# Optimization experiments

Measured on AMD Instinct MI355X. Metric: run time of the kernel, lower is better.

## Reference

```python
import jax, jax.numpy as jnp
import numpy as np

B, T, IN, H, C = 128, 128, 75, 512, 60


def setup_inputs() -> dict:
    key = jax.random.key(0)
    ks = jax.random.split(key, 40)
    def n(k, shape, s=0.05):
        return jax.random.normal(k, shape, dtype=jnp.float32) * s
    p = {}
    p["inputs"] = jax.random.normal(ks[0], (B, T, IN), dtype=jnp.float32)
    p["epoch"] = 1
    # three used LSTMCells: lstm_cell_t, lstm_cell (spatial), lstm_cell1
    i = 1
    for nm, isz in [("t", IN), ("s", IN), ("1", IN)]:
        p[f"Wih_{nm}"] = n(ks[i], (4 * H, isz)); i += 1
        p[f"Whh_{nm}"] = n(ks[i], (4 * H, H)); i += 1
        p[f"bih_{nm}"] = n(ks[i], (4 * H,)); i += 1
        p[f"bhh_{nm}"] = n(ks[i], (4 * H,)); i += 1
    p["fc_w"] = n(ks[i], (C, H)); i += 1
    p["fc_b"] = n(ks[i], (C,)); i += 1
    p["fct_w"] = n(ks[i], (H, IN)); i += 1
    p["fct_b"] = n(ks[i], (H,)); i += 1
    p["fc1_w"] = n(ks[i], (H, IN)); i += 1
    p["fc1_b"] = n(ks[i], (H,)); i += 1
    p["fc2_w"] = n(ks[i], (IN // 3, H)); i += 1
    p["fc2_b"] = n(ks[i], (IN // 3,)); i += 1
    p["W_x_t"] = n(ks[i], (H, H)); i += 1
    p["W_h_t"] = n(ks[i], (H, H)); i += 1
    p["b_t"] = n(ks[i], (H,)); i += 1
    p["W_x_s"] = n(ks[i], (H, H)); i += 1
    p["W_h_s"] = n(ks[i], (H, H)); i += 1
    p["U_s"] = n(ks[i], (H, H)); i += 1
    p["b_s"] = n(ks[i], (H,)); i += 1
    p["b_us"] = n(ks[i], (H,)); i += 1
    return p


def reference(inputs, epoch,
              Wih_t, Whh_t, bih_t, bhh_t,
              Wih_s, Whh_s, bih_s, bhh_s,
              Wih_1, Whh_1, bih_1, bhh_1,
              fc_w, fc_b, fct_w, fct_b, fc1_w, fc1_b, fc2_w, fc2_b,
              W_x_t, W_h_t, b_t, W_x_s, W_h_s, U_s, b_s, b_us):
    def cell(x, h, c, Wih, Whh, bih, bhh):
        g = x @ Wih.T + bih + h @ Whh.T + bhh            # [B, 4H]
        i, f, gg, o = jnp.split(g, 4, axis=1)
        c2 = jax.nn.sigmoid(f) * c + jax.nn.sigmoid(i) * jnp.tanh(gg)
        return jax.nn.sigmoid(o) * jnp.tanh(c2), c2

    def step(carry, x):  # x: [B, IN]
        hn_t, cn_t, hn_s, cn_s, hn1, cn1 = carry
        h_prev_t = hn_t
        hn_t, cn_t = cell(x, hn_t, cn_t, Wih_t, Whh_t, bih_t, bhh_t)
        # temporal gate beta (note: original adds BOTH b_s and b_t)
        beta = jax.nn.relu((x @ fct_w.T + fct_b) @ W_x_t + h_prev_t @ W_h_t + b_s + b_t)
        h_prev = hn_s
        hn_s, cn_s = cell(x, hn_s, cn_s, Wih_s, Whh_s, bih_s, bhh_s)
        st = jnp.tanh((x @ fc1_w.T + fc1_b) @ W_x_s + h_prev @ W_h_s + b_s)
        st = st @ U_s + b_us
        q = st @ fc2_w.T + fc2_b                          # [B, IN/3]
        alpha = jax.nn.softmax(q, axis=1)                  # exp(q)/sum(exp(q))
        x_gated = x * jnp.repeat(alpha, 3, axis=1)
        hn1, cn1 = cell(x_gated, hn1, cn1, Wih_1, Whh_1, bih_1, bhh_1)
        # torch in-place aliasing bug: zt = hn1; zt *= beta mutates hn1,
        # so the gated value is carried as the next-step hidden state.
        hn1 = hn1 * beta
        return (hn_t, cn_t, hn_s, cn_s, hn1, cn1), (hn1, alpha, beta)

    Bn, Tn = inputs.shape[0], inputs.shape[1]
    z = jnp.zeros((Bn, Whh_t.shape[1]), dtype=inputs.dtype)
    init = (z, z, z, z, z, z)
    xs = jnp.swapaxes(inputs, 0, 1)  # [T, B, IN]
    _, (outs, alphas, betas) = jax.lax.scan(step, init, xs)
    logits = outs[-1] @ fc_w.T + fc_b
    logp = jax.nn.log_softmax(logits, axis=-1)
    # original reshapes the [T, B, *] stacks directly to (B, T, -1)
    alpha_out = alphas.reshape(Bn, Tn, -1)
    beta_out = betas.reshape(Bn, Tn, -1)
    return logp, alpha_out, beta_out
```

## Files before the change

### kernel.cpp

```cpp
#include <hip/hip_runtime.h>
#include <math.h>

#define B_ 128
#define T_ 128
#define IN_ 75
#define H_ 512
#define C_ 60
#define Q_ 25

constexpr size_t OFF_WHHP = 0;
constexpr size_t OFF_WIHP = 6291456;
constexpr size_t OFF_WXHP = 7225344;
constexpr size_t OFF_FT2P = 9322496;
constexpr size_t OFF_U2   = 9478144;
constexpr size_t OFF_B2   = 9529344;
constexpr size_t OFF_ST8  = 9529472;
constexpr size_t OFF_BETA = 10709120;
constexpr size_t OFF_QP   = 10971264;
constexpr size_t OFF_FLG  = 11380864;
constexpr size_t WS_BYTES = 11397376;

#define GO_IDX 4112

struct Full {
  const float* inputs;
  const float* Wih_t; const float* Whh_t; const float* bih_t; const float* bhh_t;
  const float* Wih_s; const float* Whh_s; const float* bih_s; const float* bhh_s;
  const float* Wih_1; const float* Whh_1; const float* bih_1; const float* bhh_1;
  const float* fc_w;  const float* fc_b;
  const float* fct_w; const float* fct_b;
  const float* fc1_w; const float* fc1_b;
  const float* fc2_w; const float* fc2_b;
  const float* W_x_t; const float* W_h_t; const float* b_t;
  const float* W_x_s; const float* W_h_s; const float* U_s; const float* b_s; const float* b_us;
  char* ws; float* out;
};

typedef _Float16 h2t __attribute__((ext_vector_type(2)));
union U32H { unsigned u; h2t h; unsigned short s[2]; };

__device__ __forceinline__ float sigm(float v) { return 1.f / (1.f + expf(-v)); }
__device__ __forceinline__ float dot2(unsigned a, unsigned b, float c) {
#if __has_builtin(__builtin_amdgcn_fdot2)
  U32H A, B; A.u = a; B.u = b;
  return __builtin_amdgcn_fdot2(A.h, B.h, c, false);
#else
  U32H A, B; A.u = a; B.u = b;
  return fmaf((float)A.h.x, (float)B.h.x, fmaf((float)A.h.y, (float)B.h.y, c));
#endif
}
__device__ __forceinline__ unsigned pack2h(float a, float b) {
  U32H r; r.h.x = (_Float16)a; r.h.y = (_Float16)b; return r.u;
}
__device__ __forceinline__ unsigned short f2h(float a) {
  U32H r; r.u = 0; r.h.x = (_Float16)a; return r.s[0];
}
__device__ __forceinline__ unsigned packss(unsigned short lo, unsigned short hi) {
  return (unsigned)lo | ((unsigned)hi << 16);
}
__device__ __forceinline__ float hlo(unsigned v) { U32H r; r.u = v; return (float)r.h.x; }
__device__ __forceinline__ float hhi(unsigned v) { U32H r; r.u = v; return (float)r.h.y; }

__global__ void prep_pack(Full f) {
  uint4* WHHP = (uint4*)(f.ws + OFF_WHHP);
  uint4* WIHP = (uint4*)(f.ws + OFF_WIHP);
  unsigned* WXHP = (unsigned*)(f.ws + OFF_WXHP);
  unsigned* FT2P = (unsigned*)(f.ws + OFF_FT2P);
  float* U2 = (float*)(f.ws + OFF_U2);
  float* B2 = (float*)(f.ws + OFF_B2);
  unsigned* FLG = (unsigned*)(f.ws + OFF_FLG);
  for (int i = blockIdx.x * blockDim.x + threadIdx.x; i < 4128; i += gridDim.x * blockDim.x)
    FLG[i] = 0u;

  const size_t N1 = (size_t)3 * 256 * 512;
  const size_t N2 = (size_t)3 * 38 * 512;
  const size_t N3 = (size_t)4 * 256 * 512;
  const size_t N4 = (size_t)2 * 38 * 512;
  const size_t N5 = (size_t)25 * 512;
  const size_t N6 = 25;
  const size_t TOT = N1 + N2 + N3 + N4 + N5 + N6;
  for (size_t i = (size_t)blockIdx.x * blockDim.x + threadIdx.x; i < TOT;
       i += (size_t)gridDim.x * blockDim.x) {
    if (i < N1) {
      size_t c = i / 131072, r = i % 131072, k2 = r >> 9, u = r & 511;
      const float* W = (c == 0) ? f.Whh_t : (c == 1) ? f.Whh_s : f.Whh_1;
      uint4 v;
      v.x = pack2h(W[(0 * 512 + u) * 512 + 2 * k2], W[(0 * 512 + u) * 512 + 2 * k2 + 1]);
      v.y = pack2h(W[(1 * 512 + u) * 512 + 2 * k2], W[(1 * 512 + u) * 512 + 2 * k2 + 1]);
      v.z = pack2h(W[(2 * 512 + u) * 512 + 2 * k2], W[(2 * 512 + u) * 512 + 2 * k2 + 1]);
      v.w = pack2h(W[(3 * 512 + u) * 512 + 2 * k2], W[(3 * 512 + u) * 512 + 2 * k2 + 1]);
      WHHP[i] = v;
    } else if (i < N1 + N2) {
      size_t e = i - N1; size_t c = e / 19456, r = e % 19456, k2 = r >> 9, u = r & 511;
      const float* W = (c == 0) ? f.Wih_t : (c == 1) ? f.Wih_s : f.Wih_1;
      int k = 2 * (int)k2;
      uint4 v;
#pragma unroll
      for (int g = 0; g < 4; ++g) {
        float a = (k < 75) ? W[(g * 512 + u) * 75 + k] : 0.f;
        float b = (k + 1 < 75) ? W[(g * 512 + u) * 75 + k + 1] : 0.f;
        (&v.x)[g] = pack2h(a, b);
      }
      WIHP[e] = v;
    } else if (i < N1 + N2 + N3) {
      size_t e = i - N1 - N2; size_t w = e / 131072, r = e % 131072, k2 = r >> 9, u = r & 511;
      const float* W = (w == 0) ? f.W_x_t : (w == 1) ? f.W_h_t : (w == 2) ? f.W_x_s : f.W_h_s;
      WXHP[e] = pack2h(W[2 * k2 * 512 + u], W[(2 * k2 + 1) * 512 + u]);
    } else if (i < N1 + N2 + N3 + N4) {
      size_t e = i - N1 - N2 - N3; size_t c = e / 19456, r = e % 19456, k2 = r >> 9, u = r & 511;
      const float* W = c ? f.fc1_w : f.fct_w;
      int k = 2 * (int)k2;
      float a = (k < 75) ? W[u * 75 + k] : 0.f;
      float b = (k + 1 < 75) ? W[u * 75 + k + 1] : 0.f;
      FT2P[e] = pack2h(a, b);
    } else if (i < N1 + N2 + N3 + N4 + N5) {
      size_t e = i - N1 - N2 - N3 - N4; size_t qi = e >> 9, u = e & 511;
      float acc = 0.f;
      for (int n = 0; n < 512; ++n) acc = fmaf(f.U_s[u * 512 + n], f.fc2_w[qi * 512 + n], acc);
      U2[qi * 512 + u] = acc;
    } else {
      size_t qi = i - N1 - N2 - N3 - N4 - N5;
      float acc = f.fc2_b[qi];
      for (int n = 0; n < 512; ++n) acc = fmaf(f.b_us[n], f.fc2_w[qi * 512 + n], acc);
      B2[qi] = acc;
    }
  }
}

__global__ __launch_bounds__(512) void prep_state(Full f) {
  const int b = blockIdx.x, j = threadIdx.x;
  __shared__ float x0[77];
  __shared__ float t1L[512], t2L[512];
  if (j < IN_) x0[j] = f.inputs[(size_t)b * T_ * IN_ + j];
  __syncthreads();
  float t1 = f.fct_b[j], t2 = f.fc1_b[j];
  for (int k = 0; k < IN_; ++k) {
    t1 = fmaf(x0[k], f.fct_w[j * IN_ + k], t1);
    t2 = fmaf(x0[k], f.fc1_w[j * IN_ + k], t2);
  }
  t1L[j] = t1; t2L[j] = t2;
  __syncthreads();
  unsigned* S = (unsigned*)(f.ws + OFF_ST8);
  if (j < 256) {
    S[0 * 32768 + j * 128 + b] = 0u;
    S[2 * 32768 + j * 128 + b] = 0u;
    S[8 * 32768 + j * 128 + b] = 0u;
    S[4 * 32768 + j * 128 + b] = pack2h(t1L[2 * j], t1L[2 * j + 1]);
    S[6 * 32768 + j * 128 + b] = pack2h(t2L[2 * j], t2L[2 * j + 1]);
  }
}

__global__ __launch_bounds__(512, 4) void scan11(Full f) {
  const int tid = threadIdx.x, bid = blockIdx.x;
  const int lane = tid & 63, wave = tid >> 6;

  char* wsb = f.ws;
  const uint4* WHHP = (const uint4*)(wsb + OFF_WHHP);
  const uint4* WIHP = (const uint4*)(wsb + OFF_WIHP);
  const unsigned* WXHP = (const unsigned*)(wsb + OFF_WXHP);
  const unsigned* FT2P = (const unsigned*)(wsb + OFF_FT2P);
  const float* U2 = (const float*)(wsb + OFF_U2);
  const float* B2 = (const float*)(wsb + OFF_B2);
  unsigned* SB = (unsigned*)(wsb + OFF_ST8);
  float* BETA = (float*)(wsb + OFF_BETA);
  float* QPART = (float*)(wsb + OFF_QP);
  unsigned* FLG = (unsigned*)(wsb + OFF_FLG);

  float* out_logp = f.out;
  float* out_alpha = f.out + B_ * C_;
  float* out_beta = f.out + B_ * C_ + (size_t)T_ * B_ * Q_;

  __shared__ __align__(16) char lds[73728];

  unsigned bcount = 0;
#define GBAR() do { \
    ++bcount; \
    __syncthreads(); \
    if (tid == 0) \
      __hip_atomic_store(&FLG[bid * 16], bcount, __ATOMIC_RELEASE, __HIP_MEMORY_SCOPE_AGENT); \
    if (bid == 0) { \
      if (tid < 256) { \
        while (__hip_atomic_load(&FLG[tid * 16], __ATOMIC_RELAXED, __HIP_MEMORY_SCOPE_AGENT) < bcount) \
          __builtin_amdgcn_s_sleep(2); \
      } \
      __syncthreads(); \
      if (tid == 0) \
        __hip_atomic_store(&FLG[GO_IDX], bcount, __ATOMIC_RELEASE, __HIP_MEMORY_SCOPE_AGENT); \
    } \
    if (tid == 0) { \
      while (__hip_atomic_load(&FLG[GO_IDX], __ATOMIC_RELAXED, __HIP_MEMORY_SCOPE_AGENT) < bcount) \
        __builtin_amdgcn_s_sleep(2); \
      (void)__hip_atomic_load(&FLG[GO_IDX], __ATOMIC_ACQUIRE, __HIP_MEMORY_SCOPE_AGENT); \
    } \
    __syncthreads(); \
  } while (0)

  if (bid < 192) {
    const int grp = bid >> 6;
    const int u0 = (bid & 63) * 8;
    const int u = u0 + wave;
    const int b0 = lane, b1 = lane + 64;

    uint4* WhhL = (uint4*)lds;
    uint4* WihL = (uint4*)(lds + 32768);
    unsigned* xL = (unsigned*)(lds + 37632);
    unsigned short* hstg = (unsigned short*)(lds + 57088);
    float* qa = (float*)(lds + 59136);
    float* biasLo = (float*)(lds + 71936);

    for (int i = tid; i < 2048; i += 512) {
      int k2 = i >> 3, uu = i & 7;
      WhhL[k2 * 8 + uu] = WHHP[((size_t)grp * 256 + k2) * 512 + u0 + uu];
    }
    for (int i = tid; i < 304; i += 512) {
      int k2 = i >> 3, uu = i & 7;
      WihL[k2 * 8 + uu] = WIHP[((size_t)grp * 38 + k2) * 512 + u0 + uu];
    }
    if (tid < 32) {
      int uu = tid >> 2, g = tid & 3;
      const float* bi = (grp == 0) ? f.bih_t : (grp == 1) ? f.bih_s : f.bih_1;
      const float* bh = (grp == 0) ? f.bhh_t : (grp == 1) ? f.bhh_s : f.bhh_1;
      biasLo[uu * 4 + g] = bi[g * 512 + u0 + uu] + bh[g * 512 + u0 + uu];
    }
    __syncthreads();

    float cc0 = 0.f, cc1 = 0.f;
    float gh0 = 0, gh1 = 0, gh2 = 0, gh3 = 0, gh4 = 0, gh5 = 0, gh6 = 0, gh7 = 0;

    for (int t = 0; t < T_; ++t) {
      const int cur = t & 1;
      for (int i = tid; i < 38 * 128; i += 512) {
        int k2 = i >> 7, b = i & 127;
        float xa = f.inputs[((size_t)b * T_ + t) * IN_ + 2 * k2];
        float xb = (2 * k2 + 1 < IN_) ? f.inputs[((size_t)b * T_ + t) * IN_ + 2 * k2 + 1] : 0.f;
        xL[k2 * 128 + b] = pack2h(xa, xb);
      }
      __syncthreads();

      const unsigned* Sr = (grp == 0) ? (SB + (size_t)cur * 32768)
                        : (grp == 1) ? (SB + (size_t)(2 + cur) * 32768)
                                     : (SB + (size_t)8 * 32768);
      float a0 = 0, a1 = 0, a2 = 0, a3 = 0, a4 = 0, a5 = 0, a6 = 0, a7 = 0;
#pragma unroll 4
      for (int k2 = 0; k2 < 256; ++k2) {
        const unsigned s0 = Sr[k2 * 128 + b0];
        const unsigned s1 = Sr[k2 * 128 + b1];
        const uint4 w = WhhL[k2 * 8 + wave];
        a0 = dot2(s0, w.x, a0); a1 = dot2(s0, w.y, a1);
        a2 = dot2(s0, w.z, a2); a3 = dot2(s0, w.w, a3);
        a4 = dot2(s1, w.x, a4); a5 = dot2(s1, w.y, a5);
        a6 = dot2(s1, w.z, a6); a7 = dot2(s1, w.w, a7);
      }
      if (grp < 2) {
#pragma unroll 2
        for (int k2 = 0; k2 < 38; ++k2) {
          const unsigned x0p = xL[k2 * 128 + b0];
          const unsigned x1p = xL[k2 * 128 + b1];
          const uint4 wi = WihL[k2 * 8 + wave];
          a0 = dot2(x0p, wi.x, a0); a1 = dot2(x0p, wi.y, a1);
          a2 = dot2(x0p, wi.z, a2); a3 = dot2(x0p, wi.w, a3);
          a4 = dot2(x1p, wi.x, a4); a5 = dot2(x1p, wi.y, a5);
          a6 = dot2(x1p, wi.z, a6); a7 = dot2(x1p, wi.w, a7);
        }
        const float* bl = &biasLo[wave * 4];
        {
          const float iv = sigm(a0 + bl[0]), fv = sigm(a1 + bl[1]);
          const float gv = tanhf(a2 + bl[2]), ov = sigm(a3 + bl[3]);
          cc0 = fv * cc0 + iv * gv;
          hstg[wave * 128 + b0] = f2h(ov * tanhf(cc0));
        }
        {
          const float iv = sigm(a4 + bl[0]), fv = sigm(a5 + bl[1]);
          const float gv = tanhf(a6 + bl[2]), ov = sigm(a7 + bl[3]);
          cc1 = fv * cc1 + iv * gv;
          hstg[wave * 128 + b1] = f2h(ov * tanhf(cc1));
        }
        __syncthreads();
        unsigned* Sw = (grp == 0) ? (SB + (size_t)(cur ^ 1) * 32768)
                                  : (SB + (size_t)(2 + (cur ^ 1)) * 32768);
        {
          int p = tid >> 7, b = tid & 127;
          Sw[(u0 / 2 + p) * 128 + b] =
              packss(hstg[(2 * p) * 128 + b], hstg[(2 * p + 1) * 128 + b]);
        }
      } else {
        const float* bl = &biasLo[wave * 4];
        gh0 = a0 + bl[0]; gh1 = a1 + bl[1]; gh2 = a2 + bl[2]; gh3 = a3 + bl[3];
        gh4 = a4 + bl[0]; gh5 = a5 + bl[1]; gh6 = a6 + bl[2]; gh7 = a7 + bl[3];
      }
      GBAR();

      if (grp == 2) {
        for (int i = tid; i < 3200; i += 512) {
          int b = i / 25, qi = i - b * 25;
          float s = B2[qi];
#pragma unroll 8
          for (int s32 = 0; s32 < 32; ++s32) s += QPART[((size_t)s32 * 128 + b) * 25 + qi];
          qa[i] = s;
        }
        __syncthreads();
        if (tid < 128) {
          float* row = &qa[tid * 25];
          float m = row[0];
          for (int i2 = 1; i2 < 25; ++i2) m = fmaxf(m, row[i2]);
          float s = 0.f;
          for (int i2 = 0; i2 < 25; ++i2) { row[i2] = expf(row[i2] - m); s += row[i2]; }
          const float inv = 1.f / s;
          for (int i2 = 0; i2 < 25; ++i2) row[i2] *= inv;
        }
        __syncthreads();
        if (bid == 128) {
          for (int i = tid; i < 3200; i += 512) {
            int b = i / 25, qi = i - b * 25;
            out_alpha[((size_t)t * B_ + b) * Q_ + qi] = qa[i];
          }
        }
        float cx0 = 0, cx1 = 0, cx2 = 0, cx3 = 0, cx4 = 0, cx5 = 0, cx6 = 0, cx7 = 0;
        const float* a0r = &qa[b0 * 25];
        const float* a1r = &qa[b1 * 25];
        for (int k2 = 0; k2 < 38; ++k2) {
          const uint4 wq = WihL[k2 * 8 + wave];
          const unsigned x0p = xL[k2 * 128 + b0];
          const unsigned x1p = xL[k2 * 128 + b1];
          const int k = 2 * k2;
          const int ai0 = k / 3;
          const int ai1 = (k + 1 < IN_) ? (k + 1) / 3 : 24;
          const float xg0e = hlo(x0p) * a0r[ai0];
          const float xg0o = hhi(x0p) * a0r[ai1];
          const float xg1e = hlo(x1p) * a1r[ai0];
          const float xg1o = hhi(x1p) * a1r[ai1];
          cx0 = fmaf(xg0e, hlo(wq.x), cx0); cx0 = fmaf(xg0o, hhi(wq.x), cx0);
          cx1 = fmaf(xg0e, hlo(wq.y), cx1); cx1 = fmaf(xg0o, hhi(wq.y), cx1);
          cx2 = fmaf(xg0e, hlo(wq.z), cx2); cx2 = fmaf(xg0o, hhi(wq.z), cx2);
          cx3 = fmaf(xg0e, hlo(wq.w), cx3); cx3 = fmaf(xg0o, hhi(wq.w), cx3);
          cx4 = fmaf(xg1e, hlo(wq.x), cx4); cx4 = fmaf(xg1o, hhi(wq.x), cx4);
          cx5 = fmaf(xg1e, hlo(wq.y), cx5); cx5 = fmaf(xg1o, hhi(wq.y), cx5);
          cx6 = fmaf(xg1e, hlo(wq.z), cx6); cx6 = fmaf(xg1o, hhi(wq.z), cx6);
          cx7 = fmaf(xg1e, hlo(wq.w), cx7); cx7 = fmaf(xg1o, hhi(wq.w), cx7);
        }
        const float be0 = BETA[(size_t)u * 128 + b0];
        const float be1 = BETA[(size_t)u * 128 + b1];
        {
          const float i1 = sigm(cx0 + gh0), f1 = sigm(cx1 + gh1);
          const float g1 = tanhf(cx2 + gh2), o1 = sigm(cx3 + gh3);
          cc0 = f1 * cc0 + i1 * g1;
          hstg[wave * 128 + b0] = f2h(o1 * tanhf(cc0) * be0);
        }
        {
          const float i1 = sigm(cx4 + gh4), f1 = sigm(cx5 + gh5);
          const float g1 = tanhf(cx6 + gh6), o1 = sigm(cx7 + gh7);
          cc1 = f1 * cc1 + i1 * g1;
          hstg[wave * 128 + b1] = f2h(o1 * tanhf(cc1) * be1);
        }
        __syncthreads();
        {
          int p = tid >> 7, b = tid & 127;
          SB[(size_t)8 * 32768 + (u0 / 2 + p) * 128 + b] =
              packss(hstg[(2 * p) * 128 + b], hstg[(2 * p + 1) * 128 + b]);
        }
      }
      GBAR();
    }
  } else {
    const bool isQ = (bid >= 224);
    const int u0 = (isQ ? (bid - 224) : (bid - 192)) * 16;
    const int ub = tid >> 5, bs = tid & 31;

    unsigned* WxL = (unsigned*)lds;
    unsigned* WhL = (unsigned*)(lds + 16384);
    unsigned* fcL = (unsigned*)(lds + 32768);
    unsigned* xnL = (unsigned*)(lds + 35200);
    unsigned short* tstg = (unsigned short*)(lds + 54656);
    float* stL = (float*)(lds + 58752);
    float* biasB = (float*)(lds + 66944);

    for (int i = tid; i < 4096; i += 512) {
      int k2 = i >> 4, uu = i & 15;
      WxL[k2 * 16 + uu] = WXHP[((size_t)(isQ ? 2 : 0) * 256 + k2) * 512 + u0 + uu];
      WhL[k2 * 16 + uu] = WXHP[((size_t)(isQ ? 3 : 1) * 256 + k2) * 512 + u0 + uu];
    }
    for (int i = tid; i < 608; i += 512) {
      int k2 = i >> 4, uu = i & 15;
      fcL[k2 * 16 + uu] = FT2P[((size_t)(isQ ? 1 : 0) * 38 + k2) * 512 + u0 + uu];
    }
    if (tid < 16) {
      int g = u0 + tid;
      biasB[tid * 2] = isQ ? f.b_s[g] : (f.b_s[g] + f.b_t[g]);
      biasB[tid * 2 + 1] = isQ ? f.fc1_b[g] : f.fct_b[g];
    }
    __syncthreads();

    for (int t = 0; t < T_; ++t) {
      const int cur = t & 1;
      if (t < T_ - 1) {
        for (int i = tid; i < 38 * 128; i += 512) {
          int k2 = i >> 7, b = i & 127;
          float xa = f.inputs[((size_t)b * T_ + t + 1) * IN_ + 2 * k2];
          float xb = (2 * k2 + 1 < IN_) ? f.inputs[((size_t)b * T_ + t + 1) * IN_ + 2 * k2 + 1] : 0.f;
          xnL[k2 * 128 + b] = pack2h(xa, xb);
        }
      }
      __syncthreads();

      const unsigned* TA = SB + (size_t)((isQ ? 6 : 4) + cur) * 32768;
      const unsigned* SA = SB + (size_t)((isQ ? 2 : 0) + cur) * 32768;
      float ac0 = 0, ac1 = 0, ac2 = 0, ac3 = 0;
#pragma unroll 2
      for (int k2 = 0; k2 < 256; ++k2) {
        const unsigned wx = WxL[k2 * 16 + ub];
        const unsigned wh = WhL[k2 * 16 + ub];
        ac0 = dot2(TA[k2 * 128 + bs],      wx, ac0);
        ac1 = dot2(TA[k2 * 128 + bs + 32], wx, ac1);
        ac2 = dot2(TA[k2 * 128 + bs + 64], wx, ac2);
        ac3 = dot2(TA[k2 * 128 + bs + 96], wx, ac3);
        ac0 = dot2(SA[k2 * 128 + bs],      wh, ac0);
        ac1 = dot2(SA[k2 * 128 + bs + 32], wh, ac1);
        ac2 = dot2(SA[k2 * 128 + bs + 64], wh, ac2);
        ac3 = dot2(SA[k2 * 128 + bs + 96], wh, ac3);
      }
      const float bb0 = biasB[ub * 2];
      if (!isQ) {
        float bv;
        bv = fmaxf(ac0 + bb0, 0.f); BETA[(size_t)(u0 + ub) * 128 + bs]      = bv;
        out_beta[((size_t)t * B_ + bs) * H_ + u0 + ub] = bv;
        bv = fmaxf(ac1 + bb0, 0.f); BETA[(size_t)(u0 + ub) * 128 + bs + 32] = bv;
        out_beta[((size_t)t * B_ + bs + 32) * H_ + u0 + ub] = bv;
        bv = fmaxf(ac2 + bb0, 0.f); BETA[(size_t)(u0 + ub) * 128 + bs + 64] = bv;
        out_beta[((size_t)t * B_ + bs + 64) * H_ + u0 + ub] = bv;
        bv = fmaxf(ac3 + bb0, 0.f); BETA[(size_t)(u0 + ub) * 128 + bs + 96] = bv;
        out_beta[((size_t)t * B_ + bs + 96) * H_ + u0 + ub] = bv;
      } else {
        stL[ub * 128 + bs]      = tanhf(ac0 + bb0);
        stL[ub * 128 + bs + 32] = tanhf(ac1 + bb0);
        stL[ub * 128 + bs + 64] = tanhf(ac2 + bb0);
        stL[ub * 128 + bs + 96] = tanhf(ac3 + bb0);
      }
      float tn0 = 0, tn1 = 0, tn2 = 0, tn3 = 0;
#pragma unroll 2
      for (int k2 = 0; k2 < 38; ++k2) {
        const unsigned fc = fcL[k2 * 16 + ub];
        tn0 = dot2(xnL[k2 * 128 + bs],      fc, tn0);
        tn1 = dot2(xnL[k2 * 128 + bs + 32], fc, tn1);
        tn2 = dot2(xnL[k2 * 128 + bs + 64], fc, tn2);
        tn3 = dot2(xnL[k2 * 128 + bs + 96], fc, tn3);
      }
      const float bb1 = biasB[ub * 2 + 1];
      tstg[ub * 128 + bs]      = f2h(tn0 + bb1);
      tstg[ub * 128 + bs + 32] = f2h(tn1 + bb1);
      tstg[ub * 128 + bs + 64] = f2h(tn2 + bb1);
      tstg[ub * 128 + bs + 96] = f2h(tn3 + bb1);
      __syncthreads();
      {
        unsigned* Tw = SB + (size_t)((isQ ? 6 : 4) + (cur ^ 1)) * 32768;
        for (int i = tid; i < 1024; i += 512) {
          int p = i >> 7, b = i & 127;
          Tw[(u0 / 2 + p) * 128 + b] =
              packss(tstg[(2 * p) * 128 + b], tstg[(2 * p + 1) * 128 + b]);
        }
      }
      if (isQ) {
        const int qslice = bid - 224;
        for (int i = tid; i < 3200; i += 512) {
          int b = i / 25, qi = i - b * 25;
          float s = 0.f;
#pragma unroll
          for (int e = 0; e < 16; ++e) s = fmaf(stL[e * 128 + b], U2[(size_t)qi * 512 + u0 + e], s);
          QPART[((size_t)qslice * 128 + b) * 25 + qi] = s;
        }
      }
      GBAR();
      GBAR();
    }
  }

  if (bid < 128) {
    const int rr = bid;
    __syncthreads();
    float* hv = (float*)lds;
    float* part = hv + 512;
    float* lg = part + 480;
    {
      unsigned v = SB[(size_t)8 * 32768 + (tid >> 1) * 128 + rr];
      hv[tid] = (tid & 1) ? hhi(v) : hlo(v);
    }
    __syncthreads();
    if (tid < 480) {
      const int ci = tid >> 3, ks = tid & 7;
      const float* fr = f.fc_w + (size_t)ci * 512 + ks * 64;
      const float* hr = hv + ks * 64;
      float acc = 0.f;
      for (int j = 0; j < 64; j += 4) {
        const float4 fv = *(const float4*)(fr + j);
        const float4 hq = *(const float4*)(hr + j);
        acc += hq.x * fv.x + hq.y * fv.y + hq.z * fv.z + hq.w * fv.w;
      }
      part[ci * 8 + ks] = acc;
    }
    __syncthreads();
    if (tid < 60) {
      float s = f.fc_b[tid];
      for (int j = 0; j < 8; ++j) s += part[tid * 8 + j];
      lg[tid] = s;
    }
    __syncthreads();
    if (tid < 60) {
      float m = lg[0];
      for (int i2 = 1; i2 < 60; ++i2) m = fmaxf(m, lg[i2]);
      float ssum = 0.f;
      for (int i2 = 0; i2 < 60; ++i2) ssum += expf(lg[i2] - m);
      out_logp[(size_t)rr * C_ + tid] = lg[tid] - m - logf(ssum);
    }
  }
}

extern "C" void kernel_launch(void* const* d_in, const int* in_sizes, int n_in,
                              void* d_out, int out_size, void* d_ws, size_t ws_size,
                              hipStream_t stream) {
  if (ws_size < WS_BYTES) return;

  Full f;
  f.inputs = (const float*)d_in[0];
  f.Wih_t = (const float*)d_in[2];  f.Whh_t = (const float*)d_in[3];
  f.bih_t = (const float*)d_in[4];  f.bhh_t = (const float*)d_in[5];
  f.Wih_s = (const float*)d_in[6];  f.Whh_s = (const float*)d_in[7];
  f.bih_s = (const float*)d_in[8];  f.bhh_s = (const float*)d_in[9];
  f.Wih_1 = (const float*)d_in[10]; f.Whh_1 = (const float*)d_in[11];
  f.bih_1 = (const float*)d_in[12]; f.bhh_1 = (const float*)d_in[13];
  f.fc_w  = (const float*)d_in[14]; f.fc_b  = (const float*)d_in[15];
  f.fct_w = (const float*)d_in[16]; f.fct_b = (const float*)d_in[17];
  f.fc1_w = (const float*)d_in[18]; f.fc1_b = (const float*)d_in[19];
  f.fc2_w = (const float*)d_in[20]; f.fc2_b = (const float*)d_in[21];
  f.W_x_t = (const float*)d_in[22]; f.W_h_t = (const float*)d_in[23];
  f.b_t   = (const float*)d_in[24];
  f.W_x_s = (const float*)d_in[25]; f.W_h_s = (const float*)d_in[26];
  f.U_s   = (const float*)d_in[27]; f.b_s   = (const float*)d_in[28];
  f.b_us  = (const float*)d_in[29];
  f.ws = (char*)d_ws;
  f.out = (float*)d_out;

  hipLaunchKernelGGL(prep_pack, dim3(1024), dim3(256), 0, stream, f);
  hipLaunchKernelGGL(prep_state, dim3(128), dim3(512), 0, stream, f);

  void* args[] = { &f };
  hipLaunchCooperativeKernel((void*)scan11, dim3(256), dim3(512), args, 0, stream);
}
```

Baseline: 11.72 ms.

## Replace persistent cooperative scan with per-timestep kernel launches

The single cooperative persistent kernel, which used software grid barriers and LDS-resident weight slices, is replaced by two kernels launched per timestep (256 launches in total) plus a final logits kernel. Inputs are pre-packed to fp16 pairs in the prep kernel. Weights are now read from global memory on every step instead of being kept in LDS. The change removes the spin-barrier cost but adds kernel launch overhead and repeated global weight traffic.

```diff
diff --git a/kernel.cpp b/kernel.cpp
--- a/kernel.cpp
+++ b/kernel.cpp
@@ -14,13 +14,19 @@
 constexpr size_t OFF_FT2P = 9322496;
 constexpr size_t OFF_U2   = 9478144;
 constexpr size_t OFF_B2   = 9529344;
-constexpr size_t OFF_ST8  = 9529472;
-constexpr size_t OFF_BETA = 10709120;
-constexpr size_t OFF_QP   = 10971264;
-constexpr size_t OFF_FLG  = 11380864;
-constexpr size_t WS_BYTES = 11397376;
-
-#define GO_IDX 4112
+constexpr size_t OFF_XP   = 9529472;
+constexpr size_t OFF_HT2  = 12019840;
+constexpr size_t OFF_HS2  = 12281984;
+constexpr size_t OFF_T12  = 12544128;
+constexpr size_t OFF_T22  = 12806272;
+constexpr size_t OFF_H12  = 13068416;
+constexpr size_t OFF_CT   = 13199488;
+constexpr size_t OFF_CS   = 13461632;
+constexpr size_t OFF_C1   = 13723776;
+constexpr size_t OFF_G1H  = 13985920;
+constexpr size_t OFF_ST   = 14510208;
+constexpr size_t OFF_BETA = 14772352;
+constexpr size_t WS_BYTES = 15034496;
 
 struct Full {
   const float* inputs;
@@ -52,12 +58,6 @@
 __device__ __forceinline__ unsigned pack2h(float a, float b) {
   U32H r; r.h.x = (_Float16)a; r.h.y = (_Float16)b; return r.u;
 }
-__device__ __forceinline__ unsigned short f2h(float a) {
-  U32H r; r.u = 0; r.h.x = (_Float16)a; return r.s[0];
-}
-__device__ __forceinline__ unsigned packss(unsigned short lo, unsigned short hi) {
-  return (unsigned)lo | ((unsigned)hi << 16);
-}
 __device__ __forceinline__ float hlo(unsigned v) { U32H r; r.u = v; return (float)r.h.x; }
 __device__ __forceinline__ float hhi(unsigned v) { U32H r; r.u = v; return (float)r.h.y; }
 
@@ -68,9 +68,7 @@
   unsigned* FT2P = (unsigned*)(f.ws + OFF_FT2P);
   float* U2 = (float*)(f.ws + OFF_U2);
   float* B2 = (float*)(f.ws + OFF_B2);
-  unsigned* FLG = (unsigned*)(f.ws + OFF_FLG);
-  for (int i = blockIdx.x * blockDim.x + threadIdx.x; i < 4128; i += gridDim.x * blockDim.x)
-    FLG[i] = 0u;
+  unsigned* XP = (unsigned*)(f.ws + OFF_XP);
 
   const size_t N1 = (size_t)3 * 256 * 512;
   const size_t N2 = (size_t)3 * 38 * 512;
@@ -78,7 +76,8 @@
   const size_t N4 = (size_t)2 * 38 * 512;
   const size_t N5 = (size_t)25 * 512;
   const size_t N6 = 25;
-  const size_t TOT = N1 + N2 + N3 + N4 + N5 + N6;
+  const size_t N7 = (size_t)128 * 38 * 128;
+  const size_t TOT = N1 + N2 + N3 + N4 + N5 + N6 + N7;
   for (size_t i = (size_t)blockIdx.x * blockDim.x + threadIdx.x; i < TOT;
        i += (size_t)gridDim.x * blockDim.x) {
     if (i < N1) {
@@ -118,11 +117,19 @@
       float acc = 0.f;
       for (int n = 0; n < 512; ++n) acc = fmaf(f.U_s[u * 512 + n], f.fc2_w[qi * 512 + n], acc);
       U2[qi * 512 + u] = acc;
-    } else {
+    } else if (i < N1 + N2 + N3 + N4 + N5 + N6) {
       size_t qi = i - N1 - N2 - N3 - N4 - N5;
       float acc = f.fc2_b[qi];
       for (int n = 0; n < 512; ++n) acc = fmaf(f.b_us[n], f.fc2_w[qi * 512 + n], acc);
       B2[qi] = acc;
+    } else {
+      size_t e = i - N1 - N2 - N3 - N4 - N5 - N6;
+      size_t t = e / 4864, r = e % 4864, k2 = r >> 7, b = r & 127;
+      int k = 2 * (int)k2;
+      const size_t base = ((size_t)b * T_ + t) * IN_;
+      float xa = (k < 75) ? f.inputs[base + k] : 0.f;
+      float xb = (k + 1 < 75) ? f.inputs[base + k + 1] : 0.f;
+      XP[e] = pack2h(xa, xb);
     }
   }
 }
@@ -140,376 +147,298 @@
   }
   t1L[j] = t1; t2L[j] = t2;
   __syncthreads();
-  unsigned* S = (unsigned*)(f.ws + OFF_ST8);
+  ((float*)(f.ws + OFF_CT))[(size_t)j * 128 + b] = 0.f;
+  ((float*)(f.ws + OFF_CS))[(size_t)j * 128 + b] = 0.f;
+  ((float*)(f.ws + OFF_C1))[(size_t)j * 128 + b] = 0.f;
   if (j < 256) {
-    S[0 * 32768 + j * 128 + b] = 0u;
-    S[2 * 32768 + j * 128 + b] = 0u;
-    S[8 * 32768 + j * 128 + b] = 0u;
-    S[4 * 32768 + j * 128 + b] = pack2h(t1L[2 * j], t1L[2 * j + 1]);
-    S[6 * 32768 + j * 128 + b] = pack2h(t2L[2 * j], t2L[2 * j + 1]);
-  }
-}
-
-__global__ __launch_bounds__(512, 4) void scan11(Full f) {
+    ((unsigned*)(f.ws + OFF_HT2))[(size_t)j * 128 + b] = 0u;
+    ((unsigned*)(f.ws + OFF_HS2))[(size_t)j * 128 + b] = 0u;
+    ((unsigned*)(f.ws + OFF_H12))[(size_t)j * 128 + b] = 0u;
+    ((unsigned*)(f.ws + OFF_T12))[(size_t)j * 128 + b] = pack2h(t1L[2 * j], t1L[2 * j + 1]);
+    ((unsigned*)(f.ws + OFF_T22))[(size_t)j * 128 + b] = pack2h(t2L[2 * j], t2L[2 * j + 1]);
+  }
+}
+
+__global__ __launch_bounds__(256) void k1(Full f, int t) {
   const int tid = threadIdx.x, bid = blockIdx.x;
-  const int lane = tid & 63, wave = tid >> 6;
+  const int row = tid & 127, half = tid >> 7;
+  const int cur = t & 1;
 
   char* wsb = f.ws;
   const uint4* WHHP = (const uint4*)(wsb + OFF_WHHP);
   const uint4* WIHP = (const uint4*)(wsb + OFF_WIHP);
   const unsigned* WXHP = (const unsigned*)(wsb + OFF_WXHP);
   const unsigned* FT2P = (const unsigned*)(wsb + OFF_FT2P);
+  const unsigned* XP = (const unsigned*)(wsb + OFF_XP);
+  unsigned* HT2 = (unsigned*)(wsb + OFF_HT2);
+  unsigned* HS2 = (unsigned*)(wsb + OFF_HS2);
+  unsigned* T12 = (unsigned*)(wsb + OFF_T12);
+  unsigned* T22 = (unsigned*)(wsb + OFF_T22);
+  unsigned* H12 = (unsigned*)(wsb + OFF_H12);
+  float* CT = (float*)(wsb + OFF_CT);
+  float* CS = (float*)(wsb + OFF_CS);
+  uint4* G1H = (uint4*)(wsb + OFF_G1H);
+  float* ST = (float*)(wsb + OFF_ST);
+  float* BETA = (float*)(wsb + OFF_BETA);
+  float* out_beta = f.out + B_ * C_ + (size_t)T_ * B_ * Q_;
+
+  if (bid < 384) {
+    const int c = bid / 128;
+    const int up = (bid % 128) * 2 + half;
+    const int u0 = 2 * up, u1 = u0 + 1;
+    const unsigned* Sr = (c == 0) ? (HT2 + (size_t)cur * 32768)
+                       : (c == 1) ? (HS2 + (size_t)cur * 32768) : H12;
+    float a0 = 0, a1 = 0, a2 = 0, a3 = 0, a4 = 0, a5 = 0, a6 = 0, a7 = 0;
+#pragma unroll 4
+    for (int k2 = 0; k2 < 256; ++k2) {
+      const unsigned s = Sr[k2 * 128 + row];
+      const uint4 w0 = WHHP[((size_t)(c * 256 + k2) << 9) + u0];
+      const uint4 w1 = WHHP[((size_t)(c * 256 + k2) << 9) + u1];
+      a0 = dot2(s, w0.x, a0); a1 = dot2(s, w0.y, a1);
+      a2 = dot2(s, w0.z, a2); a3 = dot2(s, w0.w, a3);
+      a4 = dot2(s, w1.x, a4); a5 = dot2(s, w1.y, a5);
+      a6 = dot2(s, w1.z, a6); a7 = dot2(s, w1.w, a7);
+    }
+    if (c < 2) {
+#pragma unroll 2
+      for (int k2 = 0; k2 < 38; ++k2) {
+        const unsigned xp = XP[((size_t)t * 38 + k2) * 128 + row];
+        const uint4 w0 = WIHP[((size_t)(c * 38 + k2) << 9) + u0];
+        const uint4 w1 = WIHP[((size_t)(c * 38 + k2) << 9) + u1];
+        a0 = dot2(xp, w0.x, a0); a1 = dot2(xp, w0.y, a1);
+        a2 = dot2(xp, w0.z, a2); a3 = dot2(xp, w0.w, a3);
+        a4 = dot2(xp, w1.x, a4); a5 = dot2(xp, w1.y, a5);
+        a6 = dot2(xp, w1.z, a6); a7 = dot2(xp, w1.w, a7);
+      }
+      const float* bi = c ? f.bih_s : f.bih_t;
+      const float* bh = c ? f.bhh_s : f.bhh_t;
+      float* Cst = c ? CS : CT;
+      float h0, h1v;
+      {
+        const float iv = sigm(a0 + bi[u0] + bh[u0]);
+        const float fv = sigm(a1 + bi[512 + u0] + bh[512 + u0]);
+        const float gv = tanhf(a2 + bi[1024 + u0] + bh[1024 + u0]);
+        const float ov = sigm(a3 + bi[1536 + u0] + bh[1536 + u0]);
+        const float cc = fv * Cst[(size_t)u0 * 128 + row] + iv * gv;
+        Cst[(size_t)u0 * 128 + row] = cc;
+        h0 = ov * tanhf(cc);
+      }
+      {
+        const float iv = sigm(a4 + bi[u1] + bh[u1]);
+        const float fv = sigm(a5 + bi[512 + u1] + bh[512 + u1]);
+        const float gv = tanhf(a6 + bi[1024 + u1] + bh[1024 + u1]);
+        const float ov = sigm(a7 + bi[1536 + u1] + bh[1536 + u1]);
+        const float cc = fv * Cst[(size_t)u1 * 128 + row] + iv * gv;
+        Cst[(size_t)u1 * 128 + row] = cc;
+        h1v = ov * tanhf(cc);
+      }
+      unsigned* Sw = (c ? HS2 : HT2) + (size_t)(cur ^ 1) * 32768;
+      Sw[up * 128 + row] = pack2h(h0, h1v);
+    } else {
+      uint4 g;
+      g.x = pack2h(a0 + f.bih_1[u0] + f.bhh_1[u0], a4 + f.bih_1[u1] + f.bhh_1[u1]);
+      g.y = pack2h(a1 + f.bih_1[512 + u0] + f.bhh_1[512 + u0],
+                   a5 + f.bih_1[512 + u1] + f.bhh_1[512 + u1]);
+      g.z = pack2h(a2 + f.bih_1[1024 + u0] + f.bhh_1[1024 + u0],
+                   a6 + f.bih_1[1024 + u1] + f.bhh_1[1024 + u1]);
+      g.w = pack2h(a3 + f.bih_1[1536 + u0] + f.bhh_1[1536 + u0],
+                   a7 + f.bih_1[1536 + u1] + f.bhh_1[1536 + u1]);
+      G1H[(size_t)up * 128 + row] = g;
+    }
+  } else if (bid < 512) {
+    const int up = (bid - 384) * 2 + half;
+    const int u0 = 2 * up, u1 = u0 + 1;
+    const unsigned* T1r = T12 + (size_t)cur * 32768;
+    const unsigned* HTr = HT2 + (size_t)cur * 32768;
+    float aB0 = 0, aB1 = 0;
+#pragma unroll 4
+    for (int k2 = 0; k2 < 256; ++k2) {
+      const unsigned t1 = T1r[k2 * 128 + row];
+      const unsigned ht = HTr[k2 * 128 + row];
+      aB0 = dot2(t1, WXHP[((size_t)k2 << 9) + u0], aB0);
+      aB0 = dot2(ht, WXHP[((size_t)(256 + k2) << 9) + u0], aB0);
+      aB1 = dot2(t1, WXHP[((size_t)k2 << 9) + u1], aB1);
+      aB1 = dot2(ht, WXHP[((size_t)(256 + k2) << 9) + u1], aB1);
+    }
+    {
+      const float bv = fmaxf(aB0 + f.b_s[u0] + f.b_t[u0], 0.f);
+      BETA[(size_t)u0 * 128 + row] = bv;
+      out_beta[((size_t)t * B_ + row) * H_ + u0] = bv;
+    }
+    {
+      const float bv = fmaxf(aB1 + f.b_s[u1] + f.b_t[u1], 0.f);
+      BETA[(size_t)u1 * 128 + row] = bv;
+      out_beta[((size_t)t * B_ + row) * H_ + u1] = bv;
+    }
+    if (t < T_ - 1) {
+      float tn0 = 0, tn1 = 0;
+#pragma unroll 2
+      for (int k2 = 0; k2 < 38; ++k2) {
+        const unsigned xp = XP[((size_t)(t + 1) * 38 + k2) * 128 + row];
+        tn0 = dot2(xp, FT2P[((size_t)k2 << 9) + u0], tn0);
+        tn1 = dot2(xp, FT2P[((size_t)k2 << 9) + u1], tn1);
+      }
+      T12[(size_t)(cur ^ 1) * 32768 + up * 128 + row] =
+          pack2h(tn0 + f.fct_b[u0], tn1 + f.fct_b[u1]);
+    }
+  } else {
+    const int up = (bid - 512) * 2 + half;
+    const int u0 = 2 * up, u1 = u0 + 1;
+    const unsigned* T2r = T22 + (size_t)cur * 32768;
+    const unsigned* HSr = HS2 + (size_t)cur * 32768;
+    float aS0 = 0, aS1 = 0;
+#pragma unroll 4
+    for (int k2 = 0; k2 < 256; ++k2) {
+      const unsigned t2 = T2r[k2 * 128 + row];
+      const unsigned hs = HSr[k2 * 128 + row];
+      aS0 = dot2(t2, WXHP[((size_t)(512 + k2) << 9) + u0], aS0);
+      aS0 = dot2(hs, WXHP[((size_t)(768 + k2) << 9) + u0], aS0);
+      aS1 = dot2(t2, WXHP[((size_t)(512 + k2) << 9) + u1], aS1);
+      aS1 = dot2(hs, WXHP[((size_t)(768 + k2) << 9) + u1], aS1);
+    }
+    ST[(size_t)u0 * 128 + row] = tanhf(aS0 + f.b_s[u0]);
+    ST[(size_t)u1 * 128 + row] = tanhf(aS1 + f.b_s[u1]);
+    if (t < T_ - 1) {
+      float tn0 = 0, tn1 = 0;
+#pragma unroll 2
+      for (int k2 = 0; k2 < 38; ++k2) {
+        const unsigned xp = XP[((size_t)(t + 1) * 38 + k2) * 128 + row];
+        tn0 = dot2(xp, FT2P[((size_t)(38 + k2) << 9) + u0], tn0);
+        tn1 = dot2(xp, FT2P[((size_t)(38 + k2) << 9) + u1], tn1);
+      }
+      T22[(size_t)(cur ^ 1) * 32768 + up * 128 + row] =
+          pack2h(tn0 + f.fc1_b[u0], tn1 + f.fc1_b[u1]);
+    }
+  }
+}
+
+__global__ __launch_bounds__(256) void k2(Full f, int t) {
+  const int tid = threadIdx.x, row = blockIdx.x;
+  char* wsb = f.ws;
+  const uint4* WIHP = (const uint4*)(wsb + OFF_WIHP);
   const float* U2 = (const float*)(wsb + OFF_U2);
   const float* B2 = (const float*)(wsb + OFF_B2);
-  unsigned* SB = (unsigned*)(wsb + OFF_ST8);
-  float* BETA = (float*)(wsb + OFF_BETA);
-  float* QPART = (float*)(wsb + OFF_QP);
-  unsigned* FLG = (unsigned*)(wsb + OFF_FLG);
-
-  float* out_logp = f.out;
+  const float* ST = (const float*)(wsb + OFF_ST);
+  const float* BETA = (const float*)(wsb + OFF_BETA);
+  const uint4* G1H = (const uint4*)(wsb + OFF_G1H);
+  float* C1 = (float*)(wsb + OFF_C1);
+  unsigned* H12 = (unsigned*)(wsb + OFF_H12);
   float* out_alpha = f.out + B_ * C_;
-  float* out_beta = f.out + B_ * C_ + (size_t)T_ * B_ * Q_;
-
-  __shared__ __align__(16) char lds[73728];
-
-  unsigned bcount = 0;
-#define GBAR() do { \
-    ++bcount; \
-    __syncthreads(); \
-    if (tid == 0) \
-      __hip_atomic_store(&FLG[bid * 16], bcount, __ATOMIC_RELEASE, __HIP_MEMORY_SCOPE_AGENT); \
-    if (bid == 0) { \
-      if (tid < 256) { \
-        while (__hip_atomic_load(&FLG[tid * 16], __ATOMIC_RELAXED, __HIP_MEMORY_SCOPE_AGENT) < bcount) \
-          __builtin_amdgcn_s_sleep(2); \
-      } \
-      __syncthreads(); \
-      if (tid == 0) \
-        __hip_atomic_store(&FLG[GO_IDX], bcount, __ATOMIC_RELEASE, __HIP_MEMORY_SCOPE_AGENT); \
-    } \
-    if (tid == 0) { \
-      while (__hip_atomic_load(&FLG[GO_IDX], __ATOMIC_RELAXED, __HIP_MEMORY_SCOPE_AGENT) < bcount) \
-        __builtin_amdgcn_s_sleep(2); \
-      (void)__hip_atomic_load(&FLG[GO_IDX], __ATOMIC_ACQUIRE, __HIP_MEMORY_SCOPE_AGENT); \
-    } \
-    __syncthreads(); \
-  } while (0)
-
-  if (bid < 192) {
-    const int grp = bid >> 6;
-    const int u0 = (bid & 63) * 8;
-    const int u = u0 + wave;
-    const int b0 = lane, b1 = lane + 64;
-
-    uint4* WhhL = (uint4*)lds;
-    uint4* WihL = (uint4*)(lds + 32768);
-    unsigned* xL = (unsigned*)(lds + 37632);
-    unsigned short* hstg = (unsigned short*)(lds + 57088);
-    float* qa = (float*)(lds + 59136);
-    float* biasLo = (float*)(lds + 71936);
-
-    for (int i = tid; i < 2048; i += 512) {
-      int k2 = i >> 3, uu = i & 7;
-      WhhL[k2 * 8 + uu] = WHHP[((size_t)grp * 256 + k2) * 512 + u0 + uu];
-    }
-    for (int i = tid; i < 304; i += 512) {
-      int k2 = i >> 3, uu = i & 7;
-      WihL[k2 * 8 + uu] = WIHP[((size_t)grp * 38 + k2) * 512 + u0 + uu];
-    }
-    if (tid < 32) {
-      int uu = tid >> 2, g = tid & 3;
-      const float* bi = (grp == 0) ? f.bih_t : (grp == 1) ? f.bih_s : f.bih_1;
-      const float* bh = (grp == 0) ? f.bhh_t : (grp == 1) ? f.bhh_s : f.bhh_1;
-      biasLo[uu * 4 + g] = bi[g * 512 + u0 + uu] + bh[g * 512 + u0 + uu];
-    }
-    __syncthreads();
-
-    float cc0 = 0.f, cc1 = 0.f;
-    float gh0 = 0, gh1 = 0, gh2 = 0, gh3 = 0, gh4 = 0, gh5 = 0, gh6 = 0, gh7 = 0;
-
-    for (int t = 0; t < T_; ++t) {
-      const int cur = t & 1;
-      for (int i = tid; i < 38 * 128; i += 512) {
-        int k2 = i >> 7, b = i & 127;
-        float xa = f.inputs[((size_t)b * T_ + t) * IN_ + 2 * k2];
-        float xb = (2 * k2 + 1 < IN_) ? f.inputs[((size_t)b * T_ + t) * IN_ + 2 * k2 + 1] : 0.f;
-        xL[k2 * 128 + b] = pack2h(xa, xb);
-      }
-      __syncthreads();
-
-      const unsigned* Sr = (grp == 0) ? (SB + (size_t)cur * 32768)
-                        : (grp == 1) ? (SB + (size_t)(2 + cur) * 32768)
-                                     : (SB + (size_t)8 * 32768);
-      float a0 = 0, a1 = 0, a2 = 0, a3 = 0, a4 = 0, a5 = 0, a6 = 0, a7 = 0;
-#pragma unroll 4
-      for (int k2 = 0; k2 < 256; ++k2) {
-        const unsigned s0 = Sr[k2 * 128 + b0];
-        const unsigned s1 = Sr[k2 * 128 + b1];
-        const uint4 w = WhhL[k2 * 8 + wave];
-        a0 = dot2(s0, w.x, a0); a1 = dot2(s0, w.y, a1);
-        a2 = dot2(s0, w.z, a2); a3 = dot2(s0, w.w, a3);
-        a4 = dot2(s1, w.x, a4); a5 = dot2(s1, w.y, a5);
-        a6 = dot2(s1, w.z, a6); a7 = dot2(s1, w.w, a7);
-      }
-      if (grp < 2) {
+
+  __shared__ float stv[512];
+  __shared__ float qp[200];
+  __shared__ float qv[25];
+  __shared__ float al[25];
+  __shared__ unsigned xgp[40];
+
+  stv[tid] = ST[(size_t)tid * 128 + row];
+  stv[tid + 256] = ST[(size_t)(tid + 256) * 128 + row];
+  __syncthreads();
+  if (tid < 200) {
+    const int qi = tid >> 3, ks = tid & 7;
+    const float* u2p = U2 + (size_t)qi * 512 + ks * 64;
+    const float* sp = stv + ks * 64;
+    float acc = 0.f;
+    for (int j = 0; j < 64; j += 4) {
+      const float4 uv = *(const float4*)(u2p + j);
+      const float4 sv = *(const float4*)(sp + j);
+      acc += sv.x * uv.x + sv.y * uv.y + sv.z * uv.z + sv.w * uv.w;
+    }
+    qp[tid] = acc;
+  }
+  __syncthreads();
+  if (tid < 25) {
+    float s = B2[tid];
+    for (int j = 0; j < 8; ++j) s += qp[tid * 8 + j];
+    qv[tid] = s;
+  }
+  __syncthreads();
+  if (tid < 25) {
+    float m = qv[0];
+    for (int i2 = 1; i2 < 25; ++i2) m = fmaxf(m, qv[i2]);
+    float s = 0.f;
+    for (int i2 = 0; i2 < 25; ++i2) s += expf(qv[i2] - m);
+    const float a = expf(qv[tid] - m) / s;
+    al[tid] = a;
+    out_alpha[((size_t)t * B_ + row) * Q_ + tid] = a;
+  }
+  __syncthreads();
+  if (tid < 38) {
+    const int k = 2 * tid;
+    const size_t base = ((size_t)row * T_ + t) * IN_;
+    const float xa = f.inputs[base + k] * al[k / 3];
+    const float xb = (k + 1 < IN_) ? f.inputs[base + k + 1] * al[(k + 1) / 3] : 0.f;
+    xgp[tid] = pack2h(xa, xb);
+  }
+  __syncthreads();
+  const int u0 = 2 * tid, u1 = u0 + 1;
+  float c0 = 0, c1a = 0, c2 = 0, c3 = 0, c4 = 0, c5 = 0, c6 = 0, c7 = 0;
 #pragma unroll 2
-        for (int k2 = 0; k2 < 38; ++k2) {
-          const unsigned x0p = xL[k2 * 128 + b0];
-          const unsigned x1p = xL[k2 * 128 + b1];
-          const uint4 wi = WihL[k2 * 8 + wave];
-          a0 = dot2(x0p, wi.x, a0); a1 = dot2(x0p, wi.y, a1);
-          a2 = dot2(x0p, wi.z, a2); a3 = dot2(x0p, wi.w, a3);
-          a4 = dot2(x1p, wi.x, a4); a5 = dot2(x1p, wi.y, a5);
-          a6 = dot2(x1p, wi.z, a6); a7 = dot2(x1p, wi.w, a7);
-        }
-        const float* bl = &biasLo[wave * 4];
-        {
-          const float iv = sigm(a0 + bl[0]), fv = sigm(a1 + bl[1]);
-          const float gv = tanhf(a2 + bl[2]), ov = sigm(a3 + bl[3]);
-          cc0 = fv * cc0 + iv * gv;
-          hstg[wave * 128 + b0] = f2h(ov * tanhf(cc0));
-        }
-        {
-          const float iv = sigm(a4 + bl[0]), fv = sigm(a5 + bl[1]);
-          const float gv = tanhf(a6 + bl[2]), ov = sigm(a7 + bl[3]);
-          cc1 = fv * cc1 + iv * gv;
-          hstg[wave * 128 + b1] = f2h(ov * tanhf(cc1));
-        }
-        __syncthreads();
-        unsigned* Sw = (grp == 0) ? (SB + (size_t)(cur ^ 1) * 32768)
-                                  : (SB + (size_t)(2 + (cur ^ 1)) * 32768);
-        {
-          int p = tid >> 7, b = tid & 127;
-          Sw[(u0 / 2 + p) * 128 + b] =
-              packss(hstg[(2 * p) * 128 + b], hstg[(2 * p + 1) * 128 + b]);
-        }
-      } else {
-        const float* bl = &biasLo[wave * 4];
-        gh0 = a0 + bl[0]; gh1 = a1 + bl[1]; gh2 = a2 + bl[2]; gh3 = a3 + bl[3];
-        gh4 = a4 + bl[0]; gh5 = a5 + bl[1]; gh6 = a6 + bl[2]; gh7 = a7 + bl[3];
-      }
-      GBAR();
-
-      if (grp == 2) {
-        for (int i = tid; i < 3200; i += 512) {
-          int b = i / 25, qi = i - b * 25;
-          float s = B2[qi];
-#pragma unroll 8
-          for (int s32 = 0; s32 < 32; ++s32) s += QPART[((size_t)s32 * 128 + b) * 25 + qi];
-          qa[i] = s;
-        }
-        __syncthreads();
-        if (tid < 128) {
-          float* row = &qa[tid * 25];
-          float m = row[0];
-          for (int i2 = 1; i2 < 25; ++i2) m = fmaxf(m, row[i2]);
-          float s = 0.f;
-          for (int i2 = 0; i2 < 25; ++i2) { row[i2] = expf(row[i2] - m); s += row[i2]; }
-          const float inv = 1.f / s;
-          for (int i2 = 0; i2 < 25; ++i2) row[i2] *= inv;
-        }
-        __syncthreads();
-        if (bid == 128) {
-          for (int i = tid; i < 3200; i += 512) {
-            int b = i / 25, qi = i - b * 25;
-            out_alpha[((size_t)t * B_ + b) * Q_ + qi] = qa[i];
-          }
-        }
-        float cx0 = 0, cx1 = 0, cx2 = 0, cx3 = 0, cx4 = 0, cx5 = 0, cx6 = 0, cx7 = 0;
-        const float* a0r = &qa[b0 * 25];
-        const float* a1r = &qa[b1 * 25];
-        for (int k2 = 0; k2 < 38; ++k2) {
-          const uint4 wq = WihL[k2 * 8 + wave];
-          const unsigned x0p = xL[k2 * 128 + b0];
-          const unsigned x1p = xL[k2 * 128 + b1];
-          const int k = 2 * k2;
-          const int ai0 = k / 3;
-          const int ai1 = (k + 1 < IN_) ? (k + 1) / 3 : 24;
-          const float xg0e = hlo(x0p) * a0r[ai0];
-          const float xg0o = hhi(x0p) * a0r[ai1];
-          const float xg1e = hlo(x1p) * a1r[ai0];
-          const float xg1o = hhi(x1p) * a1r[ai1];
-          cx0 = fmaf(xg0e, hlo(wq.x), cx0); cx0 = fmaf(xg0o, hhi(wq.x), cx0);
-          cx1 = fmaf(xg0e, hlo(wq.y), cx1); cx1 = fmaf(xg0o, hhi(wq.y), cx1);
-          cx2 = fmaf(xg0e, hlo(wq.z), cx2); cx2 = fmaf(xg0o, hhi(wq.z), cx2);
-          cx3 = fmaf(xg0e, hlo(wq.w), cx3); cx3 = fmaf(xg0o, hhi(wq.w), cx3);
-          cx4 = fmaf(xg1e, hlo(wq.x), cx4); cx4 = fmaf(xg1o, hhi(wq.x), cx4);
-          cx5 = fmaf(xg1e, hlo(wq.y), cx5); cx5 = fmaf(xg1o, hhi(wq.y), cx5);
-          cx6 = fmaf(xg1e, hlo(wq.z), cx6); cx6 = fmaf(xg1o, hhi(wq.z), cx6);
-          cx7 = fmaf(xg1e, hlo(wq.w), cx7); cx7 = fmaf(xg1o, hhi(wq.w), cx7);
-        }
-        const float be0 = BETA[(size_t)u * 128 + b0];
-        const float be1 = BETA[(size_t)u * 128 + b1];
-        {
-          const float i1 = sigm(cx0 + gh0), f1 = sigm(cx1 + gh1);
-          const float g1 = tanhf(cx2 + gh2), o1 = sigm(cx3 + gh3);
-          cc0 = f1 * cc0 + i1 * g1;
-          hstg[wave * 128 + b0] = f2h(o1 * tanhf(cc0) * be0);
-        }
-        {
-          const float i1 = sigm(cx4 + gh4), f1 = sigm(cx5 + gh5);
-          const float g1 = tanhf(cx6 + gh6), o1 = sigm(cx7 + gh7);
-          cc1 = f1 * cc1 + i1 * g1;
-          hstg[wave * 128 + b1] = f2h(o1 * tanhf(cc1) * be1);
-        }
-        __syncthreads();
-        {
-          int p = tid >> 7, b = tid & 127;
-          SB[(size_t)8 * 32768 + (u0 / 2 + p) * 128 + b] =
-              packss(hstg[(2 * p) * 128 + b], hstg[(2 * p + 1) * 128 + b]);
-        }
-      }
-      GBAR();
-    }
-  } else {
-    const bool isQ = (bid >= 224);
-    const int u0 = (isQ ? (bid - 224) : (bid - 192)) * 16;
-    const int ub = tid >> 5, bs = tid & 31;
-
-    unsigned* WxL = (unsigned*)lds;
-    unsigned* WhL = (unsigned*)(lds + 16384);
-    unsigned* fcL = (unsigned*)(lds + 32768);
-    unsigned* xnL = (unsigned*)(lds + 35200);
-    unsigned short* tstg = (unsigned short*)(lds + 54656);
-    float* stL = (float*)(lds + 58752);
-    float* biasB = (float*)(lds + 66944);
-
-    for (int i = tid; i < 4096; i += 512) {
-      int k2 = i >> 4, uu = i & 15;
-      WxL[k2 * 16 + uu] = WXHP[((size_t)(isQ ? 2 : 0) * 256 + k2) * 512 + u0 + uu];
-      WhL[k2 * 16 + uu] = WXHP[((size_t)(isQ ? 3 : 1) * 256 + k2) * 512 + u0 + uu];
-    }
-    for (int i = tid; i < 608; i += 512) {
-      int k2 = i >> 4, uu = i & 15;
-      fcL[k2 * 16 + uu] = FT2P[((size_t)(isQ ? 1 : 0) * 38 + k2) * 512 + u0 + uu];
-    }
-    if (tid < 16) {
-      int g = u0 + tid;
-      biasB[tid * 2] = isQ ? f.b_s[g] : (f.b_s[g] + f.b_t[g]);
-      biasB[tid * 2 + 1] = isQ ? f.fc1_b[g] : f.fct_b[g];
-    }
-    __syncthreads();
-
-    for (int t = 0; t < T_; ++t) {
-      const int cur = t & 1;
-      if (t < T_ - 1) {
-        for (int i = tid; i < 38 * 128; i += 512) {
-          int k2 = i >> 7, b = i & 127;
-          float xa = f.inputs[((size_t)b * T_ + t + 1) * IN_ + 2 * k2];
-          float xb = (2 * k2 + 1 < IN_) ? f.inputs[((size_t)b * T_ + t + 1) * IN_ + 2 * k2 + 1] : 0.f;
-          xnL[k2 * 128 + b] = pack2h(xa, xb);
-        }
-      }
-      __syncthreads();
-
-      const unsigned* TA = SB + (size_t)((isQ ? 6 : 4) + cur) * 32768;
-      const unsigned* SA = SB + (size_t)((isQ ? 2 : 0) + cur) * 32768;
-      float ac0 = 0, ac1 = 0, ac2 = 0, ac3 = 0;
-#pragma unroll 2
-      for (int k2 = 0; k2 < 256; ++k2) {
-        const unsigned wx = WxL[k2 * 16 + ub];
-        const unsigned wh = WhL[k2 * 16 + ub];
-        ac0 = dot2(TA[k2 * 128 + bs],      wx, ac0);
-        ac1 = dot2(TA[k2 * 128 + bs + 32], wx, ac1);
-        ac2 = dot2(TA[k2 * 128 + bs + 64], wx, ac2);
-        ac3 = dot2(TA[k2 * 128 + bs + 96], wx, ac3);
-        ac0 = dot2(SA[k2 * 128 + bs],      wh, ac0);
-        ac1 = dot2(SA[k2 * 128 + bs + 32], wh, ac1);
-        ac2 = dot2(SA[k2 * 128 + bs + 64], wh, ac2);
-        ac3 = dot2(SA[k2 * 128 + bs + 96], wh, ac3);
-      }
-      const float bb0 = biasB[ub * 2];
-      if (!isQ) {
-        float bv;
-        bv = fmaxf(ac0 + bb0, 0.f); BETA[(size_t)(u0 + ub) * 128 + bs]      = bv;
-        out_beta[((size_t)t * B_ + bs) * H_ + u0 + ub] = bv;
-        bv = fmaxf(ac1 + bb0, 0.f); BETA[(size_t)(u0 + ub) * 128 + bs + 32] = bv;
-        out_beta[((size_t)t * B_ + bs + 32) * H_ + u0 + ub] = bv;
-        bv = fmaxf(ac2 + bb0, 0.f); BETA[(size_t)(u0 + ub) * 128 + bs + 64] = bv;
-        out_beta[((size_t)t * B_ + bs + 64) * H_ + u0 + ub] = bv;
-        bv = fmaxf(ac3 + bb0, 0.f); BETA[(size_t)(u0 + ub) * 128 + bs + 96] = bv;
-        out_beta[((size_t)t * B_ + bs + 96) * H_ + u0 + ub] = bv;
-      } else {
-        stL[ub * 128 + bs]      = tanhf(ac0 + bb0);
-        stL[ub * 128 + bs + 32] = tanhf(ac1 + bb0);
-        stL[ub * 128 + bs + 64] = tanhf(ac2 + bb0);
-        stL[ub * 128 + bs + 96] = tanhf(ac3 + bb0);
-      }
-      float tn0 = 0, tn1 = 0, tn2 = 0, tn3 = 0;
-#pragma unroll 2
-      for (int k2 = 0; k2 < 38; ++k2) {
-        const unsigned fc = fcL[k2 * 16 + ub];
-        tn0 = dot2(xnL[k2 * 128 + bs],      fc, tn0);
-        tn1 = dot2(xnL[k2 * 128 + bs + 32], fc, tn1);
-        tn2 = dot2(xnL[k2 * 128 + bs + 64], fc, tn2);
-        tn3 = dot2(xnL[k2 * 128 + bs + 96], fc, tn3);
-      }
-      const float bb1 = biasB[ub * 2 + 1];
-      tstg[ub * 128 + bs]      = f2h(tn0 + bb1);
-      tstg[ub * 128 + bs + 32] = f2h(tn1 + bb1);
-      tstg[ub * 128 + bs + 64] = f2h(tn2 + bb1);
-      tstg[ub * 128 + bs + 96] = f2h(tn3 + bb1);
-      __syncthreads();
-      {
-        unsigned* Tw = SB + (size_t)((isQ ? 6 : 4) + (cur ^ 1)) * 32768;
-        for (int i = tid; i < 1024; i += 512) {
-          int p = i >> 7, b = i & 127;
-          Tw[(u0 / 2 + p) * 128 + b] =
-              packss(tstg[(2 * p) * 128 + b], tstg[(2 * p + 1) * 128 + b]);
-        }
-      }
-      if (isQ) {
-        const int qslice = bid - 224;
-        for (int i = tid; i < 3200; i += 512) {
-          int b = i / 25, qi = i - b * 25;
-          float s = 0.f;
-#pragma unroll
-          for (int e = 0; e < 16; ++e) s = fmaf(stL[e * 128 + b], U2[(size_t)qi * 512 + u0 + e], s);
-          QPART[((size_t)qslice * 128 + b) * 25 + qi] = s;
-        }
-      }
-      GBAR();
-      GBAR();
-    }
-  }
-
-  if (bid < 128) {
-    const int rr = bid;
-    __syncthreads();
-    float* hv = (float*)lds;
-    float* part = hv + 512;
-    float* lg = part + 480;
-    {
-      unsigned v = SB[(size_t)8 * 32768 + (tid >> 1) * 128 + rr];
-      hv[tid] = (tid & 1) ? hhi(v) : hlo(v);
-    }
-    __syncthreads();
-    if (tid < 480) {
-      const int ci = tid >> 3, ks = tid & 7;
-      const float* fr = f.fc_w + (size_t)ci * 512 + ks * 64;
-      const float* hr = hv + ks * 64;
-      float acc = 0.f;
-      for (int j = 0; j < 64; j += 4) {
-        const float4 fv = *(const float4*)(fr + j);
-        const float4 hq = *(const float4*)(hr + j);
-        acc += hq.x * fv.x + hq.y * fv.y + hq.z * fv.z + hq.w * fv.w;
-      }
-      part[ci * 8 + ks] = acc;
-    }
-    __syncthreads();
-    if (tid < 60) {
-      float s = f.fc_b[tid];
-      for (int j = 0; j < 8; ++j) s += part[tid * 8 + j];
-      lg[tid] = s;
-    }
-    __syncthreads();
-    if (tid < 60) {
-      float m = lg[0];
-      for (int i2 = 1; i2 < 60; ++i2) m = fmaxf(m, lg[i2]);
-      float ssum = 0.f;
-      for (int i2 = 0; i2 < 60; ++i2) ssum += expf(lg[i2] - m);
-      out_logp[(size_t)rr * C_ + tid] = lg[tid] - m - logf(ssum);
-    }
+  for (int k2 = 0; k2 < 38; ++k2) {
+    const unsigned xp = xgp[k2];
+    const uint4 w0 = WIHP[((size_t)(2 * 38 + k2) << 9) + u0];
+    const uint4 w1 = WIHP[((size_t)(2 * 38 + k2) << 9) + u1];
+    c0 = dot2(xp, w0.x, c0); c1a = dot2(xp, w0.y, c1a);
+    c2 = dot2(xp, w0.z, c2); c3 = dot2(xp, w0.w, c3);
+    c4 = dot2(xp, w1.x, c4); c5 = dot2(xp, w1.y, c5);
+    c6 = dot2(xp, w1.z, c6); c7 = dot2(xp, w1.w, c7);
+  }
+  const uint4 g = G1H[(size_t)tid * 128 + row];
+  float h0, h1v;
+  {
+    const float i1 = sigm(c0 + hlo(g.x)), f1 = sigm(c1a + hlo(g.y));
+    const float gg = tanhf(c2 + hlo(g.z)), o1 = sigm(c3 + hlo(g.w));
+    const float cc = f1 * C1[(size_t)u0 * 128 + row] + i1 * gg;
+    C1[(size_t)u0 * 128 + row] = cc;
+    h0 = o1 * tanhf(cc) * BETA[(size_t)u0 * 128 + row];
+  }
+  {
+    const float i1 = sigm(c4 + hhi(g.x)), f1 = sigm(c5 + hhi(g.y));
+    const float gg = tanhf(c6 + hhi(g.z)), o1 = sigm(c7 + hhi(g.w));
+    const float cc = f1 * C1[(size_t)u1 * 128 + row] + i1 * gg;
+    C1[(size_t)u1 * 128 + row] = cc;
+    h1v = o1 * tanhf(cc) * BETA[(size_t)u1 * 128 + row];
+  }
+  H12[(size_t)tid * 128 + row] = pack2h(h0, h1v);
+}
+
+__global__ __launch_bounds__(256) void k3(Full f) {
+  const int tid = threadIdx.x, row = blockIdx.x;
+  const unsigned* H12 = (const unsigned*)(f.ws + OFF_H12);
+  __shared__ float hv[512];
+  __shared__ float part[240];
+  __shared__ float lg[60];
+  {
+    const unsigned v = H12[(size_t)tid * 128 + row];
+    hv[2 * tid] = hlo(v);
+    hv[2 * tid + 1] = hhi(v);
+  }
+  __syncthreads();
+  if (tid < 240) {
+    const int ci = tid >> 2, ks = tid & 3;
+    const float* fr = f.fc_w + (size_t)ci * 512 + ks * 128;
+    const float* hr = hv + ks * 128;
+    float acc = 0.f;
+    for (int j = 0; j < 128; j += 4) {
+      const float4 fv = *(const float4*)(fr + j);
+      const float4 hq = *(const float4*)(hr + j);
+      acc += hq.x * fv.x + hq.y * fv.y + hq.z * fv.z + hq.w * fv.w;
+    }
+    part[tid] = acc;
+  }
+  __syncthreads();
+  if (tid < 60) {
+    float s = f.fc_b[tid];
+    for (int j = 0; j < 4; ++j) s += part[tid * 4 + j];
+    lg[tid] = s;
+  }
+  __syncthreads();
+  if (tid < 60) {
+    float m = lg[0];
+    for (int i2 = 1; i2 < 60; ++i2) m = fmaxf(m, lg[i2]);
+    float ssum = 0.f;
+    for (int i2 = 0; i2 < 60; ++i2) ssum += expf(lg[i2] - m);
+    f.out[(size_t)row * C_ + tid] = lg[tid] - m - logf(ssum);
   }
 }
 
@@ -541,6 +470,9 @@
   hipLaunchKernelGGL(prep_pack, dim3(1024), dim3(256), 0, stream, f);
   hipLaunchKernelGGL(prep_state, dim3(128), dim3(512), 0, stream, f);
 
-  void* args[] = { &f };
-  hipLaunchCooperativeKernel((void*)scan11, dim3(256), dim3(512), args, 0, stream);
-}
+  for (int t = 0; t < T_; ++t) {
+    hipLaunchKernelGGL(k1, dim3(640), dim3(256), 0, stream, f, t);
+    hipLaunchKernelGGL(k2, dim3(128), dim3(256), 0, stream, f, t);
+  }
+  hipLaunchKernelGGL(k3, dim3(128), dim3(256), 0, stream, f);
+}
```

Result: faster. 9.808 ms (-16.3%).
